# Performance work log

Hardware: AMD Instinct MI355X
Metric: run time of the kernel (lower is better)

Reference implementation:

```python
import jax, jax.numpy as jnp
import numpy as np

NV, NE, D, NNZ = 100000, 50000, 128, 1600000
EPS = 1e-5

def _seg_mean(vals, idx, n):
    # vals: [nnz, d] gathered rows; mean-aggregate into n segments
    s = jax.ops.segment_sum(vals, idx, num_segments=n)
    c = jax.ops.segment_sum(jnp.ones((idx.shape[0], 1), vals.dtype), idx, num_segments=n)
    return s / jnp.maximum(c, 1.0)

def _linear(x, W, b):
    return x @ W.T + b

def _layer_norm(x, g, b):
    m = jnp.mean(x, axis=-1, keepdims=True)
    v = jnp.mean((x - m) ** 2, axis=-1, keepdims=True)
    return (x - m) * jax.lax.rsqrt(v + EPS) * g + b

def setup_inputs() -> dict:
    key = jax.random.key(0)
    ks = jax.random.split(key, 12)
    inp = {
        "X": jax.random.normal(ks[0], (NV, D), jnp.float32),
        "Y": jax.random.normal(ks[1], (NE, D), jnp.float32),
        "v_idx": jax.random.randint(ks[2], (NNZ,), 0, NV, jnp.int32),
        "e_idx": jax.random.randint(ks[3], (NNZ,), 0, NE, jnp.int32),
        "W_tv": jax.random.normal(ks[4], (D, D), jnp.float32) * 0.05,
        "b_tv": jnp.zeros((D,), jnp.float32),
        "W_te": jax.random.normal(ks[5], (D, D), jnp.float32) * 0.05,
        "b_te": jnp.zeros((D,), jnp.float32),
        "W_em": jax.random.normal(ks[6], (D, 2 * D), jnp.float32) * 0.05,
        "b_em": jnp.zeros((D,), jnp.float32),
        "W_vm": jax.random.normal(ks[7], (D, 2 * D), jnp.float32) * 0.05,
        "b_vm": jnp.zeros((D,), jnp.float32),
        "g_v": jnp.ones((D,), jnp.float32),
        "be_v": jnp.zeros((D,), jnp.float32),
        "g_e": jnp.ones((D,), jnp.float32),
        "be_e": jnp.zeros((D,), jnp.float32),
    }
    return inp

def reference(X, Y, v_idx, e_idx, W_tv, b_tv, W_te, b_te, W_em, b_em, W_vm, b_vm, g_v, be_v, g_e, be_e):
    X0, Y0 = X, Y
    Xp = _linear(X0, W_tv, b_tv)                       # [NV, D] theta_vertex
    # v2e aggregation (mean): gather vertex rows per incidence, reduce to edges
    msg_e = _seg_mean(Xp[v_idx], e_idx, NE)            # [NE, D]
    Ym = _linear(jnp.concatenate([Y0, msg_e], axis=-1), W_em, b_em)  # edge_merge
    Ym = _linear(Ym, W_te, b_te)                       # theta_edge
    # e2v aggregation (mean)
    msg_v = _seg_mean(Ym[e_idx], v_idx, NV)            # [NV, D]
    Xm = _linear(jnp.concatenate([X0, msg_v], axis=-1), W_vm, b_vm)  # vertex_merge
    Xo = jax.nn.relu(_layer_norm(Xm, g_v, be_v))       # dropout is identity at eval / p=0
    Yo = jax.nn.relu(_layer_norm(Ym, g_e, be_e))
    return (Xo, Yo)
```

## Files before the change

kernel.cpp:

```cpp
#include <hip/hip_runtime.h>
#include <stdint.h>

#define NVERT 100000
#define NEDGE 50000
#define DIM 128
#define NNZ_N 1600000
#define N4 (NNZ_N / 4)
#define CAP_E 96
#define NB_QTR 1563

typedef __attribute__((ext_vector_type(8))) short bf16x8;
typedef __attribute__((ext_vector_type(4))) float f32x4;

__device__ __forceinline__ unsigned short f32_to_bf16(float f) {
  union { float f; unsigned u; } v; v.f = f;
  unsigned r = v.u + 0x7fffu + ((v.u >> 16) & 1u);
  return (unsigned short)(r >> 16);
}
__device__ __forceinline__ float bf16_lo(unsigned u) {
  union { unsigned u; float f; } v; v.u = u << 16; return v.f;
}
__device__ __forceinline__ float bf16_hi(unsigned u) {
  union { unsigned u; float f; } v; v.u = u & 0xffff0000u; return v.f;
}
__device__ __forceinline__ float ldf(const void* p, long i, int bf) {
  if (bf) {
    union { unsigned u; float f; } v;
    v.u = (unsigned)((const unsigned short*)p)[i] << 16;
    return v.f;
  }
  return ((const float*)p)[i];
}
__device__ __forceinline__ bf16x8 frag_ext(const void* A, long idx, int bf) {
  if (bf) return *(const bf16x8*)((const unsigned short*)A + idx);
  const float* f = (const float*)A + idx;
  float4 f0 = *(const float4*)f, f1 = *(const float4*)(f + 4);
  bf16x8 r;
  r[0] = (short)f32_to_bf16(f0.x); r[1] = (short)f32_to_bf16(f0.y);
  r[2] = (short)f32_to_bf16(f0.z); r[3] = (short)f32_to_bf16(f0.w);
  r[4] = (short)f32_to_bf16(f1.x); r[5] = (short)f32_to_bf16(f1.y);
  r[6] = (short)f32_to_bf16(f1.z); r[7] = (short)f32_to_bf16(f1.w);
  return r;
}
__device__ __forceinline__ bf16x8 frag_f32(const float* f) {
  float4 f0 = *(const float4*)f, f1 = *(const float4*)(f + 4);
  bf16x8 r;
  r[0] = (short)f32_to_bf16(f0.x); r[1] = (short)f32_to_bf16(f0.y);
  r[2] = (short)f32_to_bf16(f0.z); r[3] = (short)f32_to_bf16(f0.w);
  r[4] = (short)f32_to_bf16(f1.x); r[5] = (short)f32_to_bf16(f1.y);
  r[6] = (short)f32_to_bf16(f1.z); r[7] = (short)f32_to_bf16(f1.w);
  return r;
}

__device__ __forceinline__ int block_flag(const unsigned short* x) {
  __shared__ int cnt;
  if (threadIdx.x == 0) cnt = 0;
  __syncthreads();
  int c = 0;
#pragma unroll
  for (int k = 0; k < 4; ++k) {
    unsigned short h = x[(threadIdx.x * 4 + k) * 2];
    int ex = (h >> 7) & 0xFF;
    c += (ex >= 100 && ex <= 140) ? 1 : 0;
  }
  atomicAdd(&cnt, c);
  __syncthreads();
  return cnt > 512;
}

__global__ __launch_bounds__(256) void prep_all(
    const unsigned short* __restrict__ Xu,
    const void* __restrict__ btv, const void* __restrict__ bvm,
    const void* __restrict__ Wtv, const void* __restrict__ Wvm,
    const void* __restrict__ Wte, const void* __restrict__ Wem,
    const void* __restrict__ bte, const void* __restrict__ bem,
    float* __restrict__ btvf, float* __restrict__ bvmf, float* __restrict__ bcf,
    unsigned short* __restrict__ Wtvb, unsigned short* __restrict__ Wvmb,
    unsigned short* __restrict__ Wcb, int* __restrict__ flag,
    int* __restrict__ cnt_e, int* __restrict__ cnt_v) {
  int b = blockIdx.x, t = threadIdx.x;
  if (b >= 321) {
    int i = (b - 321) * 256 + t;
    if (i < NEDGE) cnt_e[i] = 0;
    else if (i < NEDGE + NVERT) cnt_v[i - NEDGE] = 0;
    return;
  }
  int bf = block_flag(Xu);
  if (b == 0) {
    if (t == 0) flag[0] = bf;
    if (t < 128) btvf[t] = ldf(btv, t, bf);
    else bvmf[t - 128] = ldf(bvm, t - 128, bf);
  } else if (b < 65) {
    int i = (b - 1) * 256 + t;
    Wtvb[i] = f32_to_bf16(ldf(Wtv, i, bf));
  } else if (b < 193) {
    int i = (b - 65) * 256 + t;
    Wvmb[i] = f32_to_bf16(ldf(Wvm, i, bf));
  } else {
    int n = b - 193, k = t;
    float acc = 0.f;
    for (int j = 0; j < 128; ++j)
      acc += ldf(Wte, n * 128 + j, bf) * ldf(Wem, j * 256 + k, bf);
    Wcb[n * 256 + k] = f32_to_bf16(acc);
    if (k == 0) {
      float bb = ldf(bte, n, bf);
      for (int j = 0; j < 128; ++j) bb += ldf(Wte, n * 128 + j, bf) * ldf(bem, j, bf);
      bcf[n] = bb;
    }
  }
}

__device__ __forceinline__ void ecount_body(
    const int4* __restrict__ vi, const int4* __restrict__ ei,
    int* __restrict__ cnt_e, int* __restrict__ adj_e, int bid) {
  int i = bid * 256 + threadIdx.x;
  if (i >= N4) return;
  int4 e = ei[i], v = vi[i];
  int t;
  t = atomicAdd(&cnt_e[e.x], 1); if (t < CAP_E) adj_e[e.x * CAP_E + t] = v.x;
  t = atomicAdd(&cnt_e[e.y], 1); if (t < CAP_E) adj_e[e.y * CAP_E + t] = v.y;
  t = atomicAdd(&cnt_e[e.z], 1); if (t < CAP_E) adj_e[e.z * CAP_E + t] = v.z;
  t = atomicAdd(&cnt_e[e.w], 1); if (t < CAP_E) adj_e[e.w * CAP_E + t] = v.w;
}

__device__ __forceinline__ void vcount_body(
    const int4* __restrict__ vi, int* __restrict__ cnt_v,
    int4* __restrict__ tV, int bid) {
  int i = bid * 256 + threadIdx.x;
  if (i >= N4) return;
  int4 v = vi[i];
  int4 tv;
  tv.x = atomicAdd(&cnt_v[v.x], 1);
  tv.y = atomicAdd(&cnt_v[v.y], 1);
  tv.z = atomicAdd(&cnt_v[v.z], 1);
  tv.w = atomicAdd(&cnt_v[v.w], 1);
  tV[i] = tv;
}

__device__ __forceinline__ void wadjv_body(
    const int4* __restrict__ vi, const int4* __restrict__ ei,
    const int4* __restrict__ tV, const int* __restrict__ off_v,
    const int* __restrict__ bsum, int* __restrict__ adj_v, int bid) {
  int i = bid * 256 + threadIdx.x;
  if (i >= N4) return;
  int4 e = ei[i], v = vi[i], tv = tV[i];
  adj_v[off_v[v.x] + bsum[v.x >> 10] + tv.x] = e.x;
  adj_v[off_v[v.y] + bsum[v.y >> 10] + tv.y] = e.y;
  adj_v[off_v[v.z] + bsum[v.z >> 10] + tv.z] = e.z;
  adj_v[off_v[v.w] + bsum[v.w >> 10] + tv.w] = e.w;
}

__global__ __launch_bounds__(1024) void scan_block(const int* __restrict__ in,
                                                   int* __restrict__ out,
                                                   int* __restrict__ bsum, int n) {
  __shared__ int sd[1024];
  const int tid = threadIdx.x;
  const int i = blockIdx.x * 1024 + tid;
  int x = (i < n) ? in[i] : 0;
  sd[tid] = x;
  __syncthreads();
  int v = x;
  for (int s = 1; s < 1024; s <<= 1) {
    int t = (tid >= s) ? sd[tid - s] : 0;
    __syncthreads();
    v += t;
    sd[tid] = v;
    __syncthreads();
  }
  if (i < n) out[i] = v - x;
  if (tid == 1023) bsum[blockIdx.x] = v;
}

__global__ __launch_bounds__(1024) void scan_sums(int* __restrict__ bsum, int nb) {
  __shared__ int sd[1024];
  const int tid = threadIdx.x;
  int x = (tid < nb) ? bsum[tid] : 0;
  sd[tid] = x;
  __syncthreads();
  int v = x;
  for (int s = 1; s < 1024; s <<= 1) {
    int t = (tid >= s) ? sd[tid - s] : 0;
    __syncthreads();
    v += t;
    sd[tid] = v;
    __syncthreads();
  }
  if (tid < nb) bsum[tid] = v - x;
}

template<bool CAPMODE>
__device__ __forceinline__ void seg_body(
    const int* __restrict__ off_or_cnt, const int* __restrict__ adj,
    const unsigned short* __restrict__ tbl, float* __restrict__ out,
    int nseg, int nrows, const int* __restrict__ bsum, int total, int bid) {
  const int seg = (bid * 256 + threadIdx.x) >> 4;
  const int l = threadIdx.x & 15;
  if (seg >= nseg) return;
  int s, e, cnt;
  if (CAPMODE) {
    cnt = off_or_cnt[seg];
    s = seg * CAP_E;
    e = s + (cnt < CAP_E ? cnt : CAP_E);
  } else {
    s = off_or_cnt[seg] + bsum[seg >> 10];
    e = (seg + 1 < nseg) ? off_or_cnt[seg + 1] + bsum[(seg + 1) >> 10] : total;
    cnt = e - s;
  }
  float a0 = 0, a1 = 0, a2 = 0, a3 = 0, a4 = 0, a5 = 0, a6 = 0, a7 = 0;
#define ACC(u)                                         \
  a0 += bf16_lo(u.x); a1 += bf16_hi(u.x);              \
  a2 += bf16_lo(u.y); a3 += bf16_hi(u.y);              \
  a4 += bf16_lo(u.z); a5 += bf16_hi(u.z);              \
  a6 += bf16_lo(u.w); a7 += bf16_hi(u.w);
  int i = s;
  for (; i + 4 <= e; i += 4) {
    int r0 = adj[i], r1 = adj[i + 1], r2 = adj[i + 2], r3 = adj[i + 3];
    if ((unsigned)r0 >= (unsigned)nrows) r0 = 0;
    if ((unsigned)r1 >= (unsigned)nrows) r1 = 0;
    if ((unsigned)r2 >= (unsigned)nrows) r2 = 0;
    if ((unsigned)r3 >= (unsigned)nrows) r3 = 0;
    uint4 u0 = *(const uint4*)(tbl + (long)r0 * DIM + l * 8);
    uint4 u1 = *(const uint4*)(tbl + (long)r1 * DIM + l * 8);
    uint4 u2 = *(const uint4*)(tbl + (long)r2 * DIM + l * 8);
    uint4 u3 = *(const uint4*)(tbl + (long)r3 * DIM + l * 8);
    ACC(u0) ACC(u1) ACC(u2) ACC(u3)
  }
  for (; i < e; ++i) {
    int r = adj[i];
    if ((unsigned)r >= (unsigned)nrows) r = 0;
    uint4 u = *(const uint4*)(tbl + (long)r * DIM + l * 8);
    ACC(u)
  }
#undef ACC
  float inv = (cnt > 0) ? 1.f / (float)cnt : 0.f;
  float* op = out + (long)seg * DIM + l * 8;
  *(float4*)op       = make_float4(a0 * inv, a1 * inv, a2 * inv, a3 * inv);
  *(float4*)(op + 4) = make_float4(a4 * inv, a5 * inv, a6 * inv, a7 * inv);
}

template<int KSTEPS, bool SPLIT, bool DO_LN, bool STORE_BF16>
__device__ __forceinline__ void gemm_body(
    int bid,
    const void* __restrict__ A0, const float* __restrict__ A1,
    const unsigned short* __restrict__ Bw, const float* __restrict__ biasf,
    unsigned short* __restrict__ outb, float* __restrict__ outf,
    const void* __restrict__ gw_, const void* __restrict__ bw_,
    int M, const int* flagp) {
  constexpr int K = KSTEPS * 32;
  constexpr int KA0 = SPLIT ? 128 : K;
  const int bf = *flagp;
  const int wave = threadIdx.x >> 6;
  const int lane = threadIdx.x & 63;
  const int m0 = bid * 64 + wave * 16;
  if (m0 >= M) return;
  const int c = lane & 15;
  const int q = lane >> 4;
  const long arow = m0 + c;

  f32x4 acc[8];
#pragma unroll
  for (int t = 0; t < 8; ++t) acc[t] = (f32x4){0.f, 0.f, 0.f, 0.f};

#pragma unroll
  for (int ks = 0; ks < KSTEPS; ++ks) {
    const int kk = ks * 32 + q * 8;
    bf16x8 a;
    if (SPLIT && ks >= KSTEPS / 2) a = frag_f32(A1 + arow * 128 + (kk - 128));
    else                           a = frag_ext(A0, arow * (long)KA0 + kk, bf);
#pragma unroll
    for (int t = 0; t < 8; ++t) {
      bf16x8 b = *(const bf16x8*)(Bw + (long)(t * 16 + c) * K + kk);
      acc[t] = __builtin_amdgcn_mfma_f32_16x16x32_bf16(a, b, acc[t], 0, 0, 0);
    }
  }

#pragma unroll
  for (int t = 0; t < 8; ++t) {
    float bv = biasf[t * 16 + c];
#pragma unroll
    for (int i = 0; i < 4; ++i) acc[t][i] += bv;
  }

  if (STORE_BF16) {
#pragma unroll
    for (int t = 0; t < 8; ++t) {
      int col = t * 16 + c;
#pragma unroll
      for (int i = 0; i < 4; ++i)
        outb[(long)(m0 + q * 4 + i) * DIM + col] = f32_to_bf16(acc[t][i]);
    }
  }

  if (DO_LN) {
    float sum[4] = {0, 0, 0, 0}, sq[4] = {0, 0, 0, 0};
#pragma unroll
    for (int t = 0; t < 8; ++t)
#pragma unroll
      for (int i = 0; i < 4; ++i) { float v = acc[t][i]; sum[i] += v; sq[i] += v * v; }
#pragma unroll
    for (int m = 1; m <= 8; m <<= 1) {
#pragma unroll
      for (int i = 0; i < 4; ++i) {
        sum[i] += __shfl_xor(sum[i], m, 64);
        sq[i]  += __shfl_xor(sq[i], m, 64);
      }
    }
    float mean[4], rstd[4];
#pragma unroll
    for (int i = 0; i < 4; ++i) {
      mean[i] = sum[i] * (1.0f / 128.0f);
      float var = sq[i] * (1.0f / 128.0f) - mean[i] * mean[i];
      rstd[i] = rsqrtf(var + 1e-5f);
    }
#pragma unroll
    for (int t = 0; t < 8; ++t) {
      int col = t * 16 + c;
      float gv = ldf(gw_, col, bf), bv = ldf(bw_, col, bf);
#pragma unroll
      for (int i = 0; i < 4; ++i) {
        float v = (acc[t][i] - mean[i]) * rstd[i] * gv + bv;
        v = v > 0.f ? v : 0.f;
        outf[(long)(m0 + q * 4 + i) * DIM + col] = v;
      }
    }
  }
}

__global__ __launch_bounds__(256) void k_ecount_gemm1(
    const int4* __restrict__ vi, const int4* __restrict__ ei,
    int* __restrict__ cnt_e, int* __restrict__ adj_e,
    const void* __restrict__ X, const unsigned short* __restrict__ Wtvb,
    const float* __restrict__ btvf, unsigned short* __restrict__ Xp_b,
    const int* __restrict__ flagp) {
  if (blockIdx.x & 1)
    gemm_body<4, false, false, true>(blockIdx.x >> 1, X, nullptr, Wtvb, btvf,
                                     Xp_b, nullptr, nullptr, nullptr, NVERT, flagp);
  else
    ecount_body(vi, ei, cnt_e, adj_e, blockIdx.x >> 1);
}

__global__ __launch_bounds__(256) void k_vcount_seg1(
    const int4* __restrict__ vi, int* __restrict__ cnt_v, int4* __restrict__ tV,
    const int* __restrict__ cnt_e, const int* __restrict__ adj_e,
    const unsigned short* __restrict__ Xp_b, float* __restrict__ msg_e) {
  int r = blockIdx.x % 3, q = blockIdx.x / 3;
  if (r == 0)
    vcount_body(vi, cnt_v, tV, q);
  else
    seg_body<true>(cnt_e, adj_e, Xp_b, msg_e, NEDGE, NVERT, nullptr, 0,
                   q * 2 + (r - 1));
}

__global__ __launch_bounds__(256) void k_wadjv_gemm2(
    const int4* __restrict__ vi, const int4* __restrict__ ei,
    const int4* __restrict__ tV, const int* __restrict__ off_v,
    const int* __restrict__ bsum, int* __restrict__ adj_v,
    const void* __restrict__ Y, const float* __restrict__ msg_e,
    const unsigned short* __restrict__ Wcb, const float* __restrict__ bcf,
    unsigned short* __restrict__ Ym_b, float* __restrict__ Yo,
    const void* __restrict__ g_e, const void* __restrict__ be_e,
    const int* __restrict__ flagp) {
  int r = blockIdx.x % 3, q = blockIdx.x / 3;
  if (r == 2)
    gemm_body<8, true, true, true>(q, Y, msg_e, Wcb, bcf, Ym_b, Yo, g_e, be_e,
                                   NEDGE, flagp);
  else
    wadjv_body(vi, ei, tV, off_v, bsum, adj_v, q * 2 + r);
}

__global__ __launch_bounds__(256) void seg_mean_v(
    const int* __restrict__ off_v, const int* __restrict__ bsum,
    const int* __restrict__ adj_v, const unsigned short* __restrict__ Ym_b,
    float* __restrict__ msg_v) {
  seg_body<false>(off_v, adj_v, Ym_b, msg_v, NVERT, NEDGE, bsum, NNZ_N,
                  blockIdx.x);
}

template<int KSTEPS, bool SPLIT, bool DO_LN, bool STORE_BF16>
__global__ __launch_bounds__(256) void gemm_mfma(
    const void* __restrict__ A0, const float* __restrict__ A1,
    const unsigned short* __restrict__ Bw, const float* __restrict__ biasf,
    unsigned short* __restrict__ outb, float* __restrict__ outf,
    const void* __restrict__ gw_, const void* __restrict__ bw_,
    int M, const int* flagp) {
  gemm_body<KSTEPS, SPLIT, DO_LN, STORE_BF16>(blockIdx.x, A0, A1, Bw, biasf,
                                              outb, outf, gw_, bw_, M, flagp);
}

extern "C" void kernel_launch(void* const* d_in, const int* in_sizes, int n_in,
                              void* d_out, int out_size, void* d_ws, size_t ws_size,
                              hipStream_t stream) {
  const void* X    = d_in[0];
  const void* Y    = d_in[1];
  const int*  v_idx = (const int*)d_in[2];
  const int*  e_idx = (const int*)d_in[3];
  const void* W_tv = d_in[4];
  const void* b_tv = d_in[5];
  const void* W_te = d_in[6];
  const void* b_te = d_in[7];
  const void* W_em = d_in[8];
  const void* b_em = d_in[9];
  const void* W_vm = d_in[10];
  const void* b_vm = d_in[11];
  const void* g_v  = d_in[12];
  const void* be_v = d_in[13];
  const void* g_e  = d_in[14];
  const void* be_e = d_in[15];

  unsigned short* Xp_b = (unsigned short*)d_out;
  int*   adj_e = (int*)((char*)d_out + 25600000);
  int4*  tV4   = (int4*)((char*)d_out + 44800000);
  float* msg_e = (float*)d_out + (long)NVERT * DIM;
  float* Yo    = msg_e;
  float* msg_v = (float*)d_out;
  float* Xo    = (float*)d_out;

  char* p = (char*)d_ws;
  auto alloc = [&](size_t n) { char* r = p; p += (n + 255) & ~(size_t)255; return r; };
  int*   flag  = (int*)alloc(4);
  float* btv_f = (float*)alloc(DIM * 4);
  float* bvm_f = (float*)alloc(DIM * 4);
  float* bc_f  = (float*)alloc(DIM * 4);
  unsigned short* Wtv_b = (unsigned short*)alloc(DIM * DIM * 2);
  unsigned short* Wvm_b = (unsigned short*)alloc(2 * DIM * DIM * 2);
  unsigned short* Wc_b  = (unsigned short*)alloc(2 * DIM * DIM * 2);
  unsigned short* Ym_b  = (unsigned short*)alloc((long)NEDGE * DIM * 2);
  int* off_v  = (int*)alloc((NVERT + 1) * 4);
  int* cnt_e  = (int*)alloc(NEDGE * 4);
  int* cnt_v  = (int*)alloc(NVERT * 4);
  int* bsum_v = (int*)alloc(((NVERT + 1023) / 1024) * 4);
  int* adj_v  = (int*)alloc((long)NNZ_N * 4);

  prep_all<<<321 + (NEDGE + NVERT + 255) / 256, 256, 0, stream>>>(
      (const unsigned short*)X, b_tv, b_vm, W_tv, W_vm, W_te, W_em, b_te, b_em,
      btv_f, bvm_f, bc_f, Wtv_b, Wvm_b, Wc_b, flag, cnt_e, cnt_v);

  k_ecount_gemm1<<<2 * NB_QTR, 256, 0, stream>>>(
      (const int4*)v_idx, (const int4*)e_idx, cnt_e, adj_e,
      X, Wtv_b, btv_f, Xp_b, flag);

  k_vcount_seg1<<<3 * NB_QTR, 256, 0, stream>>>(
      (const int4*)v_idx, cnt_v, tV4, cnt_e, adj_e, Xp_b, msg_e);

  {
    int nbv = (NVERT + 1023) / 1024;
    scan_block<<<nbv, 1024, 0, stream>>>(cnt_v, off_v, bsum_v, NVERT);
    scan_sums<<<1, 1024, 0, stream>>>(bsum_v, nbv);
  }

  k_wadjv_gemm2<<<3 * ((NEDGE + 63) / 64), 256, 0, stream>>>(
      (const int4*)v_idx, (const int4*)e_idx, tV4, off_v, bsum_v, adj_v,
      Y, msg_e, Wc_b, bc_f, Ym_b, Yo, g_e, be_e, flag);

  seg_mean_v<<<(NVERT + 15) / 16, 256, 0, stream>>>(
      off_v, bsum_v, adj_v, Ym_b, msg_v);

  gemm_mfma<8, true, true, false><<<(NVERT + 63) / 64, 256, 0, stream>>>(
      X, msg_v, Wvm_b, bvm_f, nullptr, Xo, g_v, be_v, NVERT, flag);
}
```

Measured before the change: 574.7 us.

## Fuse segment-mean aggregation into merge GEMMs via LDS bf16 staging

The segment-mean aggregations for edges and vertices now write their 64-row tiles as bf16 into LDS, and the following merge GEMM with LayerNorm reads them from there in the same block. This removes the fp32 msg_e and msg_v round trips through global memory and two kernel launches. The launch plan is reshuffled: vcount now runs alongside the fused edge seg+GEMM, and the adj_v write is its own kernel. In exchange each block does sequential per-segment gathers (4 segments per 16-lane group), which lowers parallelism in the gather phase, and overlap between wadjv and gemm2 is lost.

```diff
diff --git a/kernel.cpp b/kernel.cpp
--- a/kernel.cpp
+++ b/kernel.cpp
@@ -8,6 +8,7 @@
 #define N4 (NNZ_N / 4)
 #define CAP_E 96
 #define NB_QTR 1563
+#define LDS_STRIDE 136
 
 typedef __attribute__((ext_vector_type(8))) short bf16x8;
 typedef __attribute__((ext_vector_type(4))) float f32x4;
@@ -34,15 +35,6 @@
 __device__ __forceinline__ bf16x8 frag_ext(const void* A, long idx, int bf) {
   if (bf) return *(const bf16x8*)((const unsigned short*)A + idx);
   const float* f = (const float*)A + idx;
-  float4 f0 = *(const float4*)f, f1 = *(const float4*)(f + 4);
-  bf16x8 r;
-  r[0] = (short)f32_to_bf16(f0.x); r[1] = (short)f32_to_bf16(f0.y);
-  r[2] = (short)f32_to_bf16(f0.z); r[3] = (short)f32_to_bf16(f0.w);
-  r[4] = (short)f32_to_bf16(f1.x); r[5] = (short)f32_to_bf16(f1.y);
-  r[6] = (short)f32_to_bf16(f1.z); r[7] = (short)f32_to_bf16(f1.w);
-  return r;
-}
-__device__ __forceinline__ bf16x8 frag_f32(const float* f) {
   float4 f0 = *(const float4*)f, f1 = *(const float4*)(f + 4);
   bf16x8 r;
   r[0] = (short)f32_to_bf16(f0.x); r[1] = (short)f32_to_bf16(f0.y);
@@ -137,11 +129,11 @@
   tV[i] = tv;
 }
 
-__device__ __forceinline__ void wadjv_body(
+__global__ __launch_bounds__(256) void k_wadjv(
     const int4* __restrict__ vi, const int4* __restrict__ ei,
     const int4* __restrict__ tV, const int* __restrict__ off_v,
-    const int* __restrict__ bsum, int* __restrict__ adj_v, int bid) {
-  int i = bid * 256 + threadIdx.x;
+    const int* __restrict__ bsum, int* __restrict__ adj_v) {
+  int i = blockIdx.x * 256 + threadIdx.x;
   if (i >= N4) return;
   int4 e = ei[i], v = vi[i], tv = tV[i];
   adj_v[off_v[v.x] + bsum[v.x >> 10] + tv.x] = e.x;
@@ -189,66 +181,71 @@
 }
 
 template<bool CAPMODE>
-__device__ __forceinline__ void seg_body(
-    const int* __restrict__ off_or_cnt, const int* __restrict__ adj,
-    const unsigned short* __restrict__ tbl, float* __restrict__ out,
-    int nseg, int nrows, const int* __restrict__ bsum, int total, int bid) {
-  const int seg = (bid * 256 + threadIdx.x) >> 4;
+__device__ __forceinline__ void seg_to_lds(
+    const int* __restrict__ off_or_cnt, const int* __restrict__ bsum, int total,
+    const int* __restrict__ adj, const unsigned short* __restrict__ tbl,
+    unsigned short* __restrict__ lds, int nseg, int nrows, int blk) {
+  const int g = threadIdx.x >> 4;
   const int l = threadIdx.x & 15;
-  if (seg >= nseg) return;
-  int s, e, cnt;
-  if (CAPMODE) {
-    cnt = off_or_cnt[seg];
-    s = seg * CAP_E;
-    e = s + (cnt < CAP_E ? cnt : CAP_E);
-  } else {
-    s = off_or_cnt[seg] + bsum[seg >> 10];
-    e = (seg + 1 < nseg) ? off_or_cnt[seg + 1] + bsum[(seg + 1) >> 10] : total;
-    cnt = e - s;
-  }
-  float a0 = 0, a1 = 0, a2 = 0, a3 = 0, a4 = 0, a5 = 0, a6 = 0, a7 = 0;
+#pragma unroll
+  for (int t = 0; t < 4; ++t) {
+    const int seg_local = t * 16 + g;
+    const int seg = blk * 64 + seg_local;
+    if (seg < nseg) {
+      int s, e, cnt;
+      if (CAPMODE) {
+        cnt = off_or_cnt[seg];
+        s = seg * CAP_E;
+        e = s + (cnt < CAP_E ? cnt : CAP_E);
+      } else {
+        s = off_or_cnt[seg] + bsum[seg >> 10];
+        e = (seg + 1 < nseg) ? off_or_cnt[seg + 1] + bsum[(seg + 1) >> 10] : total;
+        cnt = e - s;
+      }
+      float a0 = 0, a1 = 0, a2 = 0, a3 = 0, a4 = 0, a5 = 0, a6 = 0, a7 = 0;
 #define ACC(u)                                         \
   a0 += bf16_lo(u.x); a1 += bf16_hi(u.x);              \
   a2 += bf16_lo(u.y); a3 += bf16_hi(u.y);              \
   a4 += bf16_lo(u.z); a5 += bf16_hi(u.z);              \
   a6 += bf16_lo(u.w); a7 += bf16_hi(u.w);
-  int i = s;
-  for (; i + 4 <= e; i += 4) {
-    int r0 = adj[i], r1 = adj[i + 1], r2 = adj[i + 2], r3 = adj[i + 3];
-    if ((unsigned)r0 >= (unsigned)nrows) r0 = 0;
-    if ((unsigned)r1 >= (unsigned)nrows) r1 = 0;
-    if ((unsigned)r2 >= (unsigned)nrows) r2 = 0;
-    if ((unsigned)r3 >= (unsigned)nrows) r3 = 0;
-    uint4 u0 = *(const uint4*)(tbl + (long)r0 * DIM + l * 8);
-    uint4 u1 = *(const uint4*)(tbl + (long)r1 * DIM + l * 8);
-    uint4 u2 = *(const uint4*)(tbl + (long)r2 * DIM + l * 8);
-    uint4 u3 = *(const uint4*)(tbl + (long)r3 * DIM + l * 8);
-    ACC(u0) ACC(u1) ACC(u2) ACC(u3)
-  }
-  for (; i < e; ++i) {
-    int r = adj[i];
-    if ((unsigned)r >= (unsigned)nrows) r = 0;
-    uint4 u = *(const uint4*)(tbl + (long)r * DIM + l * 8);
-    ACC(u)
-  }
+      int i = s;
+      for (; i + 4 <= e; i += 4) {
+        int r0 = adj[i], r1 = adj[i + 1], r2 = adj[i + 2], r3 = adj[i + 3];
+        if ((unsigned)r0 >= (unsigned)nrows) r0 = 0;
+        if ((unsigned)r1 >= (unsigned)nrows) r1 = 0;
+        if ((unsigned)r2 >= (unsigned)nrows) r2 = 0;
+        if ((unsigned)r3 >= (unsigned)nrows) r3 = 0;
+        uint4 u0 = *(const uint4*)(tbl + (long)r0 * DIM + l * 8);
+        uint4 u1 = *(const uint4*)(tbl + (long)r1 * DIM + l * 8);
+        uint4 u2 = *(const uint4*)(tbl + (long)r2 * DIM + l * 8);
+        uint4 u3 = *(const uint4*)(tbl + (long)r3 * DIM + l * 8);
+        ACC(u0) ACC(u1) ACC(u2) ACC(u3)
+      }
+      for (; i < e; ++i) {
+        int r = adj[i];
+        if ((unsigned)r >= (unsigned)nrows) r = 0;
+        uint4 u = *(const uint4*)(tbl + (long)r * DIM + l * 8);
+        ACC(u)
+      }
 #undef ACC
-  float inv = (cnt > 0) ? 1.f / (float)cnt : 0.f;
-  float* op = out + (long)seg * DIM + l * 8;
-  *(float4*)op       = make_float4(a0 * inv, a1 * inv, a2 * inv, a3 * inv);
-  *(float4*)(op + 4) = make_float4(a4 * inv, a5 * inv, a6 * inv, a7 * inv);
-}
-
-template<int KSTEPS, bool SPLIT, bool DO_LN, bool STORE_BF16>
+      float inv = (cnt > 0) ? 1.f / (float)cnt : 0.f;
+      bf16x8 r;
+      r[0] = (short)f32_to_bf16(a0 * inv); r[1] = (short)f32_to_bf16(a1 * inv);
+      r[2] = (short)f32_to_bf16(a2 * inv); r[3] = (short)f32_to_bf16(a3 * inv);
+      r[4] = (short)f32_to_bf16(a4 * inv); r[5] = (short)f32_to_bf16(a5 * inv);
+      r[6] = (short)f32_to_bf16(a6 * inv); r[7] = (short)f32_to_bf16(a7 * inv);
+      *(bf16x8*)&lds[seg_local * LDS_STRIDE + l * 8] = r;
+    }
+  }
+  __syncthreads();
+}
+
+template<int KSTEPS, bool STORE_BF16>
 __device__ __forceinline__ void gemm_body(
-    int bid,
-    const void* __restrict__ A0, const float* __restrict__ A1,
+    int bid, const void* __restrict__ A0,
     const unsigned short* __restrict__ Bw, const float* __restrict__ biasf,
-    unsigned short* __restrict__ outb, float* __restrict__ outf,
-    const void* __restrict__ gw_, const void* __restrict__ bw_,
-    int M, const int* flagp) {
+    unsigned short* __restrict__ outb, int M, int bf) {
   constexpr int K = KSTEPS * 32;
-  constexpr int KA0 = SPLIT ? 128 : K;
-  const int bf = *flagp;
   const int wave = threadIdx.x >> 6;
   const int lane = threadIdx.x & 63;
   const int m0 = bid * 64 + wave * 16;
@@ -260,27 +257,22 @@
   f32x4 acc[8];
 #pragma unroll
   for (int t = 0; t < 8; ++t) acc[t] = (f32x4){0.f, 0.f, 0.f, 0.f};
-
 #pragma unroll
   for (int ks = 0; ks < KSTEPS; ++ks) {
     const int kk = ks * 32 + q * 8;
-    bf16x8 a;
-    if (SPLIT && ks >= KSTEPS / 2) a = frag_f32(A1 + arow * 128 + (kk - 128));
-    else                           a = frag_ext(A0, arow * (long)KA0 + kk, bf);
+    bf16x8 a = frag_ext(A0, arow * (long)K + kk, bf);
 #pragma unroll
     for (int t = 0; t < 8; ++t) {
       bf16x8 b = *(const bf16x8*)(Bw + (long)(t * 16 + c) * K + kk);
       acc[t] = __builtin_amdgcn_mfma_f32_16x16x32_bf16(a, b, acc[t], 0, 0, 0);
     }
   }
-
 #pragma unroll
   for (int t = 0; t < 8; ++t) {
     float bv = biasf[t * 16 + c];
 #pragma unroll
     for (int i = 0; i < 4; ++i) acc[t][i] += bv;
   }
-
   if (STORE_BF16) {
 #pragma unroll
     for (int t = 0; t < 8; ++t) {
@@ -290,38 +282,84 @@
         outb[(long)(m0 + q * 4 + i) * DIM + col] = f32_to_bf16(acc[t][i]);
     }
   }
-
-  if (DO_LN) {
-    float sum[4] = {0, 0, 0, 0}, sq[4] = {0, 0, 0, 0};
-#pragma unroll
-    for (int t = 0; t < 8; ++t)
-#pragma unroll
-      for (int i = 0; i < 4; ++i) { float v = acc[t][i]; sum[i] += v; sq[i] += v * v; }
-#pragma unroll
-    for (int m = 1; m <= 8; m <<= 1) {
-#pragma unroll
-      for (int i = 0; i < 4; ++i) {
-        sum[i] += __shfl_xor(sum[i], m, 64);
-        sq[i]  += __shfl_xor(sq[i], m, 64);
-      }
-    }
-    float mean[4], rstd[4];
-#pragma unroll
-    for (int i = 0; i < 4; ++i) {
-      mean[i] = sum[i] * (1.0f / 128.0f);
-      float var = sq[i] * (1.0f / 128.0f) - mean[i] * mean[i];
-      rstd[i] = rsqrtf(var + 1e-5f);
-    }
+}
+
+template<bool STORE_BF16>
+__device__ __forceinline__ void gemm_lds_body(
+    int bid, const void* __restrict__ A0, const unsigned short* __restrict__ lds,
+    const unsigned short* __restrict__ Bw, const float* __restrict__ biasf,
+    unsigned short* __restrict__ outb, float* __restrict__ outf,
+    const void* __restrict__ gw_, const void* __restrict__ bw_,
+    int M, int bf) {
+  constexpr int K = 256;
+  const int wave = threadIdx.x >> 6;
+  const int lane = threadIdx.x & 63;
+  const int m0 = bid * 64 + wave * 16;
+  if (m0 >= M) return;
+  const int c = lane & 15;
+  const int q = lane >> 4;
+  const long arow = m0 + c;
+  const int rloc = wave * 16 + c;
+
+  f32x4 acc[8];
+#pragma unroll
+  for (int t = 0; t < 8; ++t) acc[t] = (f32x4){0.f, 0.f, 0.f, 0.f};
+#pragma unroll
+  for (int ks = 0; ks < 8; ++ks) {
+    const int kk = ks * 32 + q * 8;
+    bf16x8 a;
+    if (ks >= 4) a = *(const bf16x8*)&lds[rloc * LDS_STRIDE + (kk - 128)];
+    else         a = frag_ext(A0, arow * 128 + kk, bf);
+#pragma unroll
+    for (int t = 0; t < 8; ++t) {
+      bf16x8 b = *(const bf16x8*)(Bw + (long)(t * 16 + c) * K + kk);
+      acc[t] = __builtin_amdgcn_mfma_f32_16x16x32_bf16(a, b, acc[t], 0, 0, 0);
+    }
+  }
+#pragma unroll
+  for (int t = 0; t < 8; ++t) {
+    float bv = biasf[t * 16 + c];
+#pragma unroll
+    for (int i = 0; i < 4; ++i) acc[t][i] += bv;
+  }
+  if (STORE_BF16) {
 #pragma unroll
     for (int t = 0; t < 8; ++t) {
       int col = t * 16 + c;
-      float gv = ldf(gw_, col, bf), bv = ldf(bw_, col, bf);
-#pragma unroll
-      for (int i = 0; i < 4; ++i) {
-        float v = (acc[t][i] - mean[i]) * rstd[i] * gv + bv;
-        v = v > 0.f ? v : 0.f;
-        outf[(long)(m0 + q * 4 + i) * DIM + col] = v;
-      }
+#pragma unroll
+      for (int i = 0; i < 4; ++i)
+        outb[(long)(m0 + q * 4 + i) * DIM + col] = f32_to_bf16(acc[t][i]);
+    }
+  }
+  float sum[4] = {0, 0, 0, 0}, sq[4] = {0, 0, 0, 0};
+#pragma unroll
+  for (int t = 0; t < 8; ++t)
+#pragma unroll
+    for (int i = 0; i < 4; ++i) { float v = acc[t][i]; sum[i] += v; sq[i] += v * v; }
+#pragma unroll
+  for (int m = 1; m <= 8; m <<= 1) {
+#pragma unroll
+    for (int i = 0; i < 4; ++i) {
+      sum[i] += __shfl_xor(sum[i], m, 64);
+      sq[i]  += __shfl_xor(sq[i], m, 64);
+    }
+  }
+  float mean[4], rstd[4];
+#pragma unroll
+  for (int i = 0; i < 4; ++i) {
+    mean[i] = sum[i] * (1.0f / 128.0f);
+    float var = sq[i] * (1.0f / 128.0f) - mean[i] * mean[i];
+    rstd[i] = rsqrtf(var + 1e-5f);
+  }
+#pragma unroll
+  for (int t = 0; t < 8; ++t) {
+    int col = t * 16 + c;
+    float gv = ldf(gw_, col, bf), bv = ldf(bw_, col, bf);
+#pragma unroll
+    for (int i = 0; i < 4; ++i) {
+      float v = (acc[t][i] - mean[i]) * rstd[i] * gv + bv;
+      v = v > 0.f ? v : 0.f;
+      outf[(long)(m0 + q * 4 + i) * DIM + col] = v;
     }
   }
 }
@@ -333,58 +371,40 @@
     const float* __restrict__ btvf, unsigned short* __restrict__ Xp_b,
     const int* __restrict__ flagp) {
   if (blockIdx.x & 1)
-    gemm_body<4, false, false, true>(blockIdx.x >> 1, X, nullptr, Wtvb, btvf,
-                                     Xp_b, nullptr, nullptr, nullptr, NVERT, flagp);
+    gemm_body<4, true>(blockIdx.x >> 1, X, Wtvb, btvf, Xp_b, NVERT, *flagp);
   else
     ecount_body(vi, ei, cnt_e, adj_e, blockIdx.x >> 1);
 }
 
-__global__ __launch_bounds__(256) void k_vcount_seg1(
+__global__ __launch_bounds__(256) void k_vcount_seg1gemm2(
     const int4* __restrict__ vi, int* __restrict__ cnt_v, int4* __restrict__ tV,
     const int* __restrict__ cnt_e, const int* __restrict__ adj_e,
-    const unsigned short* __restrict__ Xp_b, float* __restrict__ msg_e) {
+    const unsigned short* __restrict__ Xp_b,
+    const void* __restrict__ Y, const unsigned short* __restrict__ Wcb,
+    const float* __restrict__ bcf, unsigned short* __restrict__ Ym_b,
+    float* __restrict__ Yo, const void* __restrict__ g_e,
+    const void* __restrict__ be_e, const int* __restrict__ flagp) {
+  __shared__ unsigned short lds[64 * LDS_STRIDE];
   int r = blockIdx.x % 3, q = blockIdx.x / 3;
-  if (r == 0)
-    vcount_body(vi, cnt_v, tV, q);
-  else
-    seg_body<true>(cnt_e, adj_e, Xp_b, msg_e, NEDGE, NVERT, nullptr, 0,
-                   q * 2 + (r - 1));
-}
-
-__global__ __launch_bounds__(256) void k_wadjv_gemm2(
-    const int4* __restrict__ vi, const int4* __restrict__ ei,
-    const int4* __restrict__ tV, const int* __restrict__ off_v,
-    const int* __restrict__ bsum, int* __restrict__ adj_v,
-    const void* __restrict__ Y, const float* __restrict__ msg_e,
-    const unsigned short* __restrict__ Wcb, const float* __restrict__ bcf,
-    unsigned short* __restrict__ Ym_b, float* __restrict__ Yo,
-    const void* __restrict__ g_e, const void* __restrict__ be_e,
-    const int* __restrict__ flagp) {
-  int r = blockIdx.x % 3, q = blockIdx.x / 3;
-  if (r == 2)
-    gemm_body<8, true, true, true>(q, Y, msg_e, Wcb, bcf, Ym_b, Yo, g_e, be_e,
-                                   NEDGE, flagp);
-  else
-    wadjv_body(vi, ei, tV, off_v, bsum, adj_v, q * 2 + r);
-}
-
-__global__ __launch_bounds__(256) void seg_mean_v(
+  if (r < 2) {
+    vcount_body(vi, cnt_v, tV, q * 2 + r);
+    return;
+  }
+  seg_to_lds<true>(cnt_e, nullptr, 0, adj_e, Xp_b, lds, NEDGE, NVERT, q);
+  gemm_lds_body<true>(q, Y, lds, Wcb, bcf, Ym_b, Yo, g_e, be_e, NEDGE, *flagp);
+}
+
+__global__ __launch_bounds__(256) void k_seg2gemm3(
     const int* __restrict__ off_v, const int* __restrict__ bsum,
     const int* __restrict__ adj_v, const unsigned short* __restrict__ Ym_b,
-    float* __restrict__ msg_v) {
-  seg_body<false>(off_v, adj_v, Ym_b, msg_v, NVERT, NEDGE, bsum, NNZ_N,
-                  blockIdx.x);
-}
-
-template<int KSTEPS, bool SPLIT, bool DO_LN, bool STORE_BF16>
-__global__ __launch_bounds__(256) void gemm_mfma(
-    const void* __restrict__ A0, const float* __restrict__ A1,
-    const unsigned short* __restrict__ Bw, const float* __restrict__ biasf,
-    unsigned short* __restrict__ outb, float* __restrict__ outf,
-    const void* __restrict__ gw_, const void* __restrict__ bw_,
-    int M, const int* flagp) {
-  gemm_body<KSTEPS, SPLIT, DO_LN, STORE_BF16>(blockIdx.x, A0, A1, Bw, biasf,
-                                              outb, outf, gw_, bw_, M, flagp);
+    const void* __restrict__ X, const unsigned short* __restrict__ Wvmb,
+    const float* __restrict__ bvmf, float* __restrict__ Xo,
+    const void* __restrict__ g_v, const void* __restrict__ be_v,
+    const int* __restrict__ flagp) {
+  __shared__ unsigned short lds[64 * LDS_STRIDE];
+  seg_to_lds<false>(off_v, bsum, NNZ_N, adj_v, Ym_b, lds, NVERT, NEDGE, blockIdx.x);
+  gemm_lds_body<false>(blockIdx.x, X, lds, Wvmb, bvmf, nullptr, Xo, g_v, be_v,
+                       NVERT, *flagp);
 }
 
 extern "C" void kernel_launch(void* const* d_in, const int* in_sizes, int n_in,
@@ -410,9 +430,7 @@
   unsigned short* Xp_b = (unsigned short*)d_out;
   int*   adj_e = (int*)((char*)d_out + 25600000);
   int4*  tV4   = (int4*)((char*)d_out + 44800000);
-  float* msg_e = (float*)d_out + (long)NVERT * DIM;
-  float* Yo    = msg_e;
-  float* msg_v = (float*)d_out;
+  float* Yo    = (float*)d_out + (long)NVERT * DIM;
   float* Xo    = (float*)d_out;
 
   char* p = (char*)d_ws;
@@ -439,8 +457,9 @@
       (const int4*)v_idx, (const int4*)e_idx, cnt_e, adj_e,
       X, Wtv_b, btv_f, Xp_b, flag);
 
-  k_vcount_seg1<<<3 * NB_QTR, 256, 0, stream>>>(
-      (const int4*)v_idx, cnt_v, tV4, cnt_e, adj_e, Xp_b, msg_e);
+  k_vcount_seg1gemm2<<<3 * ((NEDGE + 63) / 64), 256, 0, stream>>>(
+      (const int4*)v_idx, cnt_v, tV4, cnt_e, adj_e, Xp_b,
+      Y, Wc_b, bc_f, Ym_b, Yo, g_e, be_e, flag);
 
   {
     int nbv = (NVERT + 1023) / 1024;
@@ -448,13 +467,9 @@
     scan_sums<<<1, 1024, 0, stream>>>(bsum_v, nbv);
   }
 
-  k_wadjv_gemm2<<<3 * ((NEDGE + 63) / 64), 256, 0, stream>>>(
-      (const int4*)v_idx, (const int4*)e_idx, tV4, off_v, bsum_v, adj_v,
-      Y, msg_e, Wc_b, bc_f, Ym_b, Yo, g_e, be_e, flag);
-
-  seg_mean_v<<<(NVERT + 15) / 16, 256, 0, stream>>>(
-      off_v, bsum_v, adj_v, Ym_b, msg_v);
-
-  gemm_mfma<8, true, true, false><<<(NVERT + 63) / 64, 256, 0, stream>>>(
-      X, msg_v, Wvm_b, bvm_f, nullptr, Xo, g_v, be_v, NVERT, flag);
-}
+  k_wadjv<<<NB_QTR, 256, 0, stream>>>(
+      (const int4*)v_idx, (const int4*)e_idx, tV4, off_v, bsum_v, adj_v);
+
+  k_seg2gemm3<<<(NVERT + 63) / 64, 256, 0, stream>>>(
+      off_v, bsum_v, adj_v, Ym_b, X, Wvm_b, bvm_f, Xo, g_v, be_v, flag);
+}
```

New measurement: 580.7 us. No clear change (+1.0%).
